# Kernel optimization log

Hardware: AMD Instinct MI355X
Metric: run time of the kernel (lower is better)

## Reference

```python
import jax, jax.numpy as jnp
import numpy as np

N = 30000      # num_nodes
E = 480000     # num_edges
NF = 128       # node_features
EF = 64        # edge_features
HID = 256      # hidden_dim
L = 4          # num_layers
H = 8          # heads
D = HID // H   # per-head dim = 32
SCALE = 0.02


def _ln(x, g, b, eps=1e-5):
    m = x.mean(-1, keepdims=True)
    v = ((x - m) ** 2).mean(-1, keepdims=True)
    return (x - m) * jax.lax.rsqrt(v + eps) * g + b


def _mlp_head(x, W1, b1, W2, b2):
    return jax.nn.sigmoid(jax.nn.relu(x @ W1 + b1) @ W2 + b2)


def setup_inputs() -> dict:
    key = jax.random.key(0)
    ks = jax.random.split(key, 32)
    r = lambda k, shp: SCALE * jax.random.normal(k, shp, dtype=jnp.float32)
    inp = {
        'x': jax.random.normal(ks[0], (N, NF), dtype=jnp.float32),
        'edge_attr': jax.random.normal(ks[1], (E, EF), dtype=jnp.float32),
        'edge_index': jax.random.randint(ks[2], (2, E), 0, N, dtype=jnp.int32),
        # encoders
        'enc_Wn': r(ks[3], (NF, HID)), 'enc_bn': jnp.zeros((HID,), jnp.float32),
        'enc_We': r(ks[4], (EF, HID)), 'enc_be': jnp.zeros((HID,), jnp.float32),
        # stacked TransformerConv params for L layers
        'Wq': r(ks[5], (L, HID, HID)), 'bq': jnp.zeros((L, HID), jnp.float32),
        'Wk': r(ks[6], (L, HID, HID)), 'bk': jnp.zeros((L, HID), jnp.float32),
        'Wv': r(ks[7], (L, HID, HID)), 'bv': jnp.zeros((L, HID), jnp.float32),
        'We': r(ks[8], (L, HID, HID)),  # lin_edge has no bias in PyG
        'Wsk': r(ks[9], (L, HID, HID)), 'bsk': jnp.zeros((L, HID), jnp.float32),
        # shared LayerNorm (module reuses self.norm every layer)
        'ln_g': jnp.ones((HID,), jnp.float32), 'ln_b': jnp.zeros((HID,), jnp.float32),
        # contagion predictor
        'cp_W1': r(ks[10], (HID, HID // 2)), 'cp_b1': jnp.zeros((HID // 2,), jnp.float32),
        'cp_W2': r(ks[11], (HID // 2, 1)), 'cp_b2': jnp.zeros((1,), jnp.float32),
        # systemic risk predictor
        'sp_W1': r(ks[12], (HID, HID // 2)), 'sp_b1': jnp.zeros((HID // 2,), jnp.float32),
        'sp_W2': r(ks[13], (HID // 2, 1)), 'sp_b2': jnp.zeros((1,), jnp.float32),
    }
    return inp


def reference(x, edge_attr, edge_index, enc_Wn, enc_bn, enc_We, enc_be,
              Wq, bq, Wk, bk, Wv, bv, We, Wsk, bsk, ln_g, ln_b,
              cp_W1, cp_b1, cp_W2, cp_b2, sp_W1, sp_b1, sp_W2, sp_b2):
    src, dst = edge_index[0], edge_index[1]
    h = x @ enc_Wn + enc_bn                 # [N,HID]
    e = edge_attr @ enc_We + enc_be         # [E,HID]
    inv_sqrt_d = 1.0 / jnp.sqrt(jnp.asarray(D, h.dtype))
    for l in range(L):
        # TransformerConv: query at dst, key/value at src, edge bias on both k and v
        q = (h @ Wq[l] + bq[l]).reshape(N, H, D)[dst]            # [E,H,D]
        ke = (e @ We[l]).reshape(E, H, D)                        # [E,H,D]
        k = (h @ Wk[l] + bk[l]).reshape(N, H, D)[src] + ke
        v = (h @ Wv[l] + bv[l]).reshape(N, H, D)[src] + ke
        score = (q * k).sum(-1) * inv_sqrt_d                     # [E,H]
        smax = jax.ops.segment_max(score, dst, num_segments=N)   # [N,H]
        p = jnp.exp(score - smax[dst])
        denom = jax.ops.segment_sum(p, dst, num_segments=N)
        alpha = p / (denom[dst] + 1e-16)                         # scatter-softmax
        agg = jax.ops.segment_sum(alpha[..., None] * v, dst, num_segments=N)
        out = agg.reshape(N, HID) + h @ Wsk[l] + bsk[l]          # concat heads + root skip
        h = _ln(h + out, ln_g, ln_b)                             # residual + shared LN (eval: no dropout)
    g = h.mean(0, keepdims=True)                                 # [1,HID] global mean pool
    contagion_risk = _mlp_head(h, cp_W1, cp_b1, cp_W2, cp_b2)    # [N,1]
    systemic_risk = _mlp_head(g, sp_W1, sp_b1, sp_W2, sp_b2)     # [1,1]
    return h, g, contagion_risk, systemic_risk
```

## Files before the change

kernel.cpp:

```cpp
#include <hip/hip_runtime.h>
#include <cstddef>
#include <cstdint>

#define NN 30000
#define EE 480000
#define NFD 128
#define EFD 64
#define HID 256
#define NL 4
#define NH 8

#define DT_BF16 0
#define DT_F32  1
#define DT_EXT  2

#define OFF_WT  ((size_t)65787648)
#define MIN_B   ((size_t)68015872)
#define MIN_A   ((size_t)129455872)

#define WT_ENC 0
#define WT_LAYER(l) (32768 + (size_t)(l) * 262144)
#define WT_CP1 (32768 + (size_t)1048576)

typedef short bf16x8 __attribute__((ext_vector_type(8)));
typedef unsigned short us8 __attribute__((ext_vector_type(8)));
typedef float f32x4 __attribute__((ext_vector_type(4)));

__device__ __forceinline__ float bf2f(unsigned short u) {
  union { unsigned int i; float f; } v; v.i = ((unsigned int)u) << 16; return v.f;
}
__device__ __forceinline__ unsigned short f2bf(float f) {
  union { float f; unsigned int i; } v; v.f = f;
  unsigned int i = v.i;
  return (unsigned short)((i + 0x7FFFu + ((i >> 16) & 1u)) >> 16);
}
struct F4 { float x, y, z, w; };
__device__ __forceinline__ F4 load4bf(const unsigned short* p) {
  ushort4 u = *reinterpret_cast<const ushort4*>(p);
  F4 f; f.x = bf2f(u.x); f.y = bf2f(u.y); f.z = bf2f(u.z); f.w = bf2f(u.w);
  return f;
}
__device__ __forceinline__ F4 load4f(const float* p) {
  float4 t = *reinterpret_cast<const float4*>(p);
  F4 f; f.x = t.x; f.y = t.y; f.z = t.z; f.w = t.w; return f;
}
__device__ __forceinline__ F4 load4any(const void* p, size_t idx, int f32) {
  return f32 ? load4f((const float*)p + idx) : load4bf((const unsigned short*)p + idx);
}
__device__ __forceinline__ float load1any(const void* p, size_t idx, int f32) {
  return f32 ? ((const float*)p)[idx] : bf2f(((const unsigned short*)p)[idx]);
}
__device__ __forceinline__ void store1any(void* p, size_t idx, float v, int f32) {
  if (f32) ((float*)p)[idx] = v; else ((unsigned short*)p)[idx] = f2bf(v);
}

__global__ void probe_dtype(const void* __restrict__ ln_g, int* __restrict__ flag) {
  unsigned int u = *(const unsigned int*)ln_g;
  *flag = ((u & 0xFFFFu) == 0u) ? 1 : 0;
}

__global__ void wt_build(const void* __restrict__ enc_Wn,
                         const void* __restrict__ Wq, const void* __restrict__ Wk,
                         const void* __restrict__ Wv, const void* __restrict__ Wsk,
                         const void* __restrict__ cp_W1,
                         unsigned short* __restrict__ Wt, const int* __restrict__ flagp)
{
  const int f = *flagp;
  size_t idx = (size_t)blockIdx.x * 256 + threadIdx.x;
  if (idx < 32768) {
    int n = idx >> 7, k = idx & 127;
    Wt[WT_ENC + idx] = f2bf(load1any(enc_Wn, (size_t)k * 256 + n, f));
  } else if (idx < 32768 + 1048576) {
    size_t off = idx - 32768;
    int l = off >> 18;
    int which = (off >> 16) & 3;
    size_t e = off & 65535;
    int n = e >> 8, k = e & 255;
    const void* W = (which == 0) ? Wq : (which == 1) ? Wk : (which == 2) ? Wv : Wsk;
    Wt[idx] = f2bf(load1any(W, (size_t)l * 65536 + (size_t)k * 256 + n, f));
  } else if (idx < 32768 + 1048576 + 32768) {
    size_t e = idx - 32768 - 1048576;
    int n = e >> 8, k = e & 255;
    Wt[idx] = f2bf(load1any(cp_W1, (size_t)k * 128 + n, f));
  }
}

template<bool OUT_F32, bool RELU>
__global__ __launch_bounds__(256) void mfma_gemm(
    const void* __restrict__ Av, int aMode,
    const unsigned short* __restrict__ Bt,
    const void* __restrict__ biasv, size_t biasEl, int biasMode,
    void* __restrict__ Cv, int ldC, int cOff,
    int M, int K, const int* __restrict__ flagp)
{
  const int f = *flagp;
  const int aF32 = (aMode == DT_EXT) ? f : aMode;
  const int biF32 = (biasMode == DT_EXT) ? f : biasMode;

  __shared__ unsigned short Al[128][40];
  __shared__ unsigned short Bl[64][40];
  const int bm = blockIdx.x * 128;
  const int bn = blockIdx.y * 64;
  const int tid = threadIdx.x;
  const int wv = tid >> 6, lane = tid & 63;
  const int l16 = lane & 15, quad = lane >> 4;

  f32x4 acc[2][4];
#pragma unroll
  for (int i = 0; i < 2; i++)
#pragma unroll
    for (int j = 0; j < 4; j++) acc[i][j] = (f32x4){0.f, 0.f, 0.f, 0.f};

  const int ar = tid >> 1;
  const int ah = (tid & 1) << 4;
  const int bnr = tid >> 2;
  const int bk8 = (tid & 3) << 3;

  for (int k0 = 0; k0 < K; k0 += 32) {
    us8 w0, w1;
    int gr = bm + ar;
    if (gr < M) {
      if (!aF32) {
        const unsigned short* ap = (const unsigned short*)Av + (size_t)gr * K + k0 + ah;
        w0 = *(const us8*)ap;
        w1 = *(const us8*)(ap + 8);
      } else {
        const float* ap = (const float*)Av + (size_t)gr * K + k0 + ah;
        float4 u0 = *(const float4*)ap;
        float4 u1 = *(const float4*)(ap + 4);
        float4 u2 = *(const float4*)(ap + 8);
        float4 u3 = *(const float4*)(ap + 12);
        w0[0] = f2bf(u0.x); w0[1] = f2bf(u0.y); w0[2] = f2bf(u0.z); w0[3] = f2bf(u0.w);
        w0[4] = f2bf(u1.x); w0[5] = f2bf(u1.y); w0[6] = f2bf(u1.z); w0[7] = f2bf(u1.w);
        w1[0] = f2bf(u2.x); w1[1] = f2bf(u2.y); w1[2] = f2bf(u2.z); w1[3] = f2bf(u2.w);
        w1[4] = f2bf(u3.x); w1[5] = f2bf(u3.y); w1[6] = f2bf(u3.z); w1[7] = f2bf(u3.w);
      }
    } else {
      w0 = (us8)0; w1 = (us8)0;
    }
    *(us8*)&Al[ar][ah] = w0;
    *(us8*)&Al[ar][ah + 8] = w1;
    *(us8*)&Bl[bnr][bk8] = *(const us8*)&Bt[(size_t)(bn + bnr) * K + k0 + bk8];
    __syncthreads();

    bf16x8 a0 = *(const bf16x8*)&Al[wv * 32 + l16][quad * 8];
    bf16x8 a1 = *(const bf16x8*)&Al[wv * 32 + 16 + l16][quad * 8];
#pragma unroll
    for (int tn = 0; tn < 4; tn++) {
      bf16x8 b = *(const bf16x8*)&Bl[tn * 16 + l16][quad * 8];
      acc[0][tn] = __builtin_amdgcn_mfma_f32_16x16x32_bf16(a0, b, acc[0][tn], 0, 0, 0);
      acc[1][tn] = __builtin_amdgcn_mfma_f32_16x16x32_bf16(a1, b, acc[1][tn], 0, 0, 0);
    }
    __syncthreads();
  }

#pragma unroll
  for (int tm = 0; tm < 2; tm++) {
#pragma unroll
    for (int tn = 0; tn < 4; tn++) {
      int col = bn + tn * 16 + l16;
      float bias = load1any(biasv, biasEl + col, biF32);
#pragma unroll
      for (int r = 0; r < 4; r++) {
        int row = bm + wv * 32 + tm * 16 + quad * 4 + r;
        if (row < M) {
          float v = acc[tm][tn][r] + bias;
          if (RELU) v = fmaxf(v, 0.f);
          size_t off = (size_t)row * ldC + cOff + col;
          if (OUT_F32) ((float*)Cv)[off] = v;
          else ((unsigned short*)Cv)[off] = f2bf(v);
        }
      }
    }
  }
}

__global__ __launch_bounds__(256) void mfma_gemm_qkvs(
    const unsigned short* __restrict__ A,
    const unsigned short* __restrict__ Bt,
    const void* __restrict__ bq, const void* __restrict__ bk,
    const void* __restrict__ bv, const void* __restrict__ bsk, size_t biasEl,
    unsigned short* __restrict__ Qb, unsigned short* __restrict__ KVb,
    unsigned short* __restrict__ Sb,
    int M, const int* __restrict__ flagp)
{
  const int f = *flagp;
  __shared__ unsigned short Al[128][40];
  __shared__ unsigned short Bl[64][40];
  const int bm = blockIdx.x * 128;
  const int bnG = blockIdx.y * 64;
  const int which = bnG >> 8;
  const int bn = bnG & 255;
  const int tid = threadIdx.x;
  const int wv = tid >> 6, lane = tid & 63;
  const int l16 = lane & 15, quad = lane >> 4;

  f32x4 acc[2][4];
#pragma unroll
  for (int i = 0; i < 2; i++)
#pragma unroll
    for (int j = 0; j < 4; j++) acc[i][j] = (f32x4){0.f, 0.f, 0.f, 0.f};

  const int ar = tid >> 1;
  const int ah = (tid & 1) << 4;
  const int bnr = tid >> 2;
  const int bk8 = (tid & 3) << 3;
  const unsigned short* Bbase = Bt + (size_t)which * 65536;

  for (int k0 = 0; k0 < HID; k0 += 32) {
    us8 w0, w1;
    int gr = bm + ar;
    if (gr < M) {
      const unsigned short* ap = A + (size_t)gr * HID + k0 + ah;
      w0 = *(const us8*)ap;
      w1 = *(const us8*)(ap + 8);
    } else {
      w0 = (us8)0; w1 = (us8)0;
    }
    *(us8*)&Al[ar][ah] = w0;
    *(us8*)&Al[ar][ah + 8] = w1;
    *(us8*)&Bl[bnr][bk8] = *(const us8*)&Bbase[(size_t)(bn + bnr) * HID + k0 + bk8];
    __syncthreads();

    bf16x8 a0 = *(const bf16x8*)&Al[wv * 32 + l16][quad * 8];
    bf16x8 a1 = *(const bf16x8*)&Al[wv * 32 + 16 + l16][quad * 8];
#pragma unroll
    for (int tn = 0; tn < 4; tn++) {
      bf16x8 b = *(const bf16x8*)&Bl[tn * 16 + l16][quad * 8];
      acc[0][tn] = __builtin_amdgcn_mfma_f32_16x16x32_bf16(a0, b, acc[0][tn], 0, 0, 0);
      acc[1][tn] = __builtin_amdgcn_mfma_f32_16x16x32_bf16(a1, b, acc[1][tn], 0, 0, 0);
    }
    __syncthreads();
  }

  const void* biasv = (which == 0) ? bq : (which == 1) ? bk : (which == 2) ? bv : bsk;
  unsigned short* out = (which == 0) ? Qb : (which == 3) ? Sb : KVb;
  const int ldC = (which == 1 || which == 2) ? 512 : 256;
  const int cOff = (which == 2) ? 256 : 0;

#pragma unroll
  for (int tm = 0; tm < 2; tm++) {
#pragma unroll
    for (int tn = 0; tn < 4; tn++) {
      int col = bn + tn * 16 + l16;
      float bias = load1any(biasv, biasEl + col, f);
#pragma unroll
      for (int r = 0; r < 4; r++) {
        int row = bm + wv * 32 + tm * 16 + quad * 4 + r;
        if (row < M)
          out[(size_t)row * ldC + cOff + col] = f2bf(acc[tm][tn][r] + bias);
      }
    }
  }
}

__global__ void fold_kernel(const void* __restrict__ enc_We,
                            const void* __restrict__ enc_be,
                            const void* __restrict__ We_all,
                            float* __restrict__ Mfold, const int* __restrict__ flagp)
{
  const int f = *flagp;
  int idx = blockIdx.x * blockDim.x + threadIdx.x;
  if (idx >= NL * 65 * HID) return;
  int l = idx / (65 * HID);
  int rc = idx - l * 65 * HID;
  int row = rc >> 8;
  int col = rc & 255;
  size_t Wbase = (size_t)l * HID * HID;
  float acc = 0.f;
  if (row < 64) {
    for (int k = 0; k < HID; k++)
      acc += load1any(enc_We, (size_t)row * HID + k, f) * load1any(We_all, Wbase + (size_t)k * HID + col, f);
  } else {
    for (int k = 0; k < HID; k++)
      acc += load1any(enc_be, k, f) * load1any(We_all, Wbase + (size_t)k * HID + col, f);
  }
  Mfold[idx] = acc;
}

__global__ void hist_kernel(const int* __restrict__ dst, int* __restrict__ rp) {
  int e = blockIdx.x * 256 + threadIdx.x;
  if (e < EE) atomicAdd(&rp[dst[e]], 1);
}

__global__ __launch_bounds__(1024) void scan_kernel(int* __restrict__ rp) {
  __shared__ int part[1024];
  int t = threadIdx.x;
  int base = t * 30;
  int loc[30];
  int sum = 0;
#pragma unroll
  for (int i = 0; i < 30; i++) {
    int idx = base + i;
    int v = (idx < NN) ? rp[idx] : 0;
    loc[i] = v; sum += v;
  }
  part[t] = sum;
  __syncthreads();
  for (int off = 1; off < 1024; off <<= 1) {
    int v = (t >= off) ? part[t - off] : 0;
    __syncthreads();
    part[t] += v;
    __syncthreads();
  }
  int run = (t == 0) ? 0 : part[t - 1];
#pragma unroll
  for (int i = 0; i < 30; i++) {
    int idx = base + i;
    if (idx < NN) { rp[idx] = run; run += loc[i]; }
    else if (idx == NN) { rp[NN] = run; }
  }
}

__global__ void scatter_kernel(const int* __restrict__ src, const int* __restrict__ dst,
                               const int* __restrict__ rp, int* __restrict__ cnt2,
                               int2* __restrict__ sed) {
  int e = blockIdx.x * 256 + threadIdx.x;
  if (e >= EE) return;
  int d = dst[e];
  int pos = rp[d] + atomicAdd(&cnt2[d], 1);
  int2 v; v.x = src[e]; v.y = e;
  sed[pos] = v;
}

__global__ void deg_hist(const int* __restrict__ rp, int* __restrict__ dh) {
  int n = blockIdx.x * 256 + threadIdx.x;
  if (n < NN) {
    int d = rp[n + 1] - rp[n]; if (d > 255) d = 255;
    atomicAdd(&dh[d], 1);
  }
}
__global__ __launch_bounds__(256) void deg_scan(const int* __restrict__ dh,
                                                int* __restrict__ dcnt) {
  __shared__ int h[256];
  int t = threadIdx.x;
  h[t] = dh[t];
  __syncthreads();
  int s = 0;
  for (int d = t + 1; d < 256; d++) s += h[d];
  dcnt[t] = s;
}
__global__ void deg_scatter(const int* __restrict__ rp, int* __restrict__ dcnt,
                            int* __restrict__ perm) {
  int n = blockIdx.x * 256 + threadIdx.x;
  if (n < NN) {
    int d = rp[n + 1] - rp[n]; if (d > 255) d = 255;
    int pos = atomicAdd(&dcnt[d], 1);
    perm[pos] = n;
  }
}

__global__ void ea_build(const int2* __restrict__ sed, const void* __restrict__ edge_attr,
                         unsigned short* __restrict__ ea_srt, const int* __restrict__ flagp) {
  const int f = *flagp;
  int gid = blockIdx.x * 256 + threadIdx.x;
  int pos = gid >> 4;
  int sub = (gid & 15) * 4;
  int e = sed[pos].y;
  F4 v = load4any(edge_attr, (size_t)e * EFD + sub, f);
  ushort4 o; o.x = f2bf(v.x); o.y = f2bf(v.y); o.z = f2bf(v.z); o.w = f2bf(v.w);
  *reinterpret_cast<ushort4*>(ea_srt + (size_t)pos * EFD + sub) = o;
}

template<bool SORTED>
__global__ __launch_bounds__(256) void edge_fused(
    const int* __restrict__ rp, const int2* __restrict__ sed,
    const int* __restrict__ perm,
    const unsigned short* __restrict__ Qb, const unsigned short* __restrict__ KV,
    const unsigned short* __restrict__ ea_srt,
    const void* __restrict__ edge_attr,
    const float* __restrict__ Mf,
    const unsigned short* __restrict__ Sb,
    unsigned short* __restrict__ hb,
    const void* __restrict__ ln_g, const void* __restrict__ ln_b,
    const int* __restrict__ flagp)
{
  __shared__ float wl[4][8][68];
  const int f = *flagp;
  const int wv = threadIdx.x >> 6;
  const int nw = perm[blockIdx.x * 4 + wv];
  const int lane = threadIdx.x & 63;
  const int hd = lane >> 3;
  const int j = lane & 7;
  const int c4 = lane * 4;

  const size_t rowb = (size_t)nw * HID;
  F4 q4 = load4bf(Qb + rowb + c4);

  float q32[32];
#pragma unroll
  for (int i = 0; i < 8; i++) {
    F4 t = load4bf(Qb + rowb + hd * 32 + i * 4);
    q32[i * 4 + 0] = t.x; q32[i * 4 + 1] = t.y; q32[i * 4 + 2] = t.z; q32[i * 4 + 3] = t.w;
  }
  float t8[8];
#pragma unroll
  for (int kk = 0; kk < 8; kk++) {
    const float* Mrow = Mf + (size_t)(j * 8 + kk) * HID + hd * 32;
    float a = 0.f;
#pragma unroll
    for (int cc = 0; cc < 8; cc++) {
      float4 m4 = *reinterpret_cast<const float4*>(Mrow + cc * 4);
      a = fmaf(m4.x, q32[cc * 4 + 0], a);
      a = fmaf(m4.y, q32[cc * 4 + 1], a);
      a = fmaf(m4.z, q32[cc * 4 + 2], a);
      a = fmaf(m4.w, q32[cc * 4 + 3], a);
    }
    t8[kk] = a;
  }
  F4 b4 = load4f(Mf + (size_t)64 * HID + c4);
  float s0 = q4.x * b4.x + q4.y * b4.y + q4.z * b4.z + q4.w * b4.w;
  s0 += __shfl_xor(s0, 1);
  s0 += __shfl_xor(s0, 2);
  s0 += __shfl_xor(s0, 4);

  float accv[4] = {0.f, 0.f, 0.f, 0.f};
  float wacc[8] = {0.f, 0.f, 0.f, 0.f, 0.f, 0.f, 0.f, 0.f};
  float den = 0.f;
  const int beg = rp[nw], end = rp[nw + 1];

  if (beg < end) {
    const float scl = 0.17677669529663687f;
    int tA = beg;
    int tB = (beg + 1 < end) ? beg + 1 : beg;
    int sA = sed[tA].x;
    int sB = sed[tB].x;
    const unsigned short* kvp;
    kvp = KV + (size_t)sA * 512;
    F4 kA = load4bf(kvp + c4);
    F4 vA = load4bf(kvp + 256 + c4);
    kvp = KV + (size_t)sB * 512;
    F4 kB = load4bf(kvp + c4);
    F4 vB = load4bf(kvp + 256 + c4);
    F4 ea0A, ea1A, ea0B, ea1B;
    if (SORTED) {
      ea0A = load4bf(ea_srt + (size_t)tA * EFD + j * 8);
      ea1A = load4bf(ea_srt + (size_t)tA * EFD + j * 8 + 4);
      ea0B = load4bf(ea_srt + (size_t)tB * EFD + j * 8);
      ea1B = load4bf(ea_srt + (size_t)tB * EFD + j * 8 + 4);
    } else {
      size_t eA = (size_t)sed[tA].y, eB = (size_t)sed[tB].y;
      ea0A = load4any(edge_attr, eA * EFD + j * 8, f);
      ea1A = load4any(edge_attr, eA * EFD + j * 8 + 4, f);
      ea0B = load4any(edge_attr, eB * EFD + j * 8, f);
      ea1B = load4any(edge_attr, eB * EFD + j * 8 + 4, f);
    }
    int tC = (beg + 2 < end) ? beg + 2 : beg;
    int tD = (beg + 3 < end) ? beg + 3 : beg;
    int sC = sed[tC].x;
    int sD = sed[tD].x;

    for (int t = beg; t < end; t += 2) {
      kvp = KV + (size_t)sC * 512;
      F4 kC = load4bf(kvp + c4);
      F4 vC = load4bf(kvp + 256 + c4);
      kvp = KV + (size_t)sD * 512;
      F4 kD = load4bf(kvp + c4);
      F4 vD = load4bf(kvp + 256 + c4);
      F4 ea0C, ea1C, ea0D, ea1D;
      if (SORTED) {
        ea0C = load4bf(ea_srt + (size_t)tC * EFD + j * 8);
        ea1C = load4bf(ea_srt + (size_t)tC * EFD + j * 8 + 4);
        ea0D = load4bf(ea_srt + (size_t)tD * EFD + j * 8);
        ea1D = load4bf(ea_srt + (size_t)tD * EFD + j * 8 + 4);
      } else {
        size_t eC = (size_t)sed[tC].y, eD = (size_t)sed[tD].y;
        ea0C = load4any(edge_attr, eC * EFD + j * 8, f);
        ea1C = load4any(edge_attr, eC * EFD + j * 8 + 4, f);
        ea0D = load4any(edge_attr, eD * EFD + j * 8, f);
        ea1D = load4any(edge_attr, eD * EFD + j * 8 + 4, f);
      }
      int tE = (t + 4 < end) ? t + 4 : beg;
      int tF = (t + 5 < end) ? t + 5 : beg;
      int sE = sed[tE].x;
      int sF = sed[tF].x;

      float mB = (t + 1 < end) ? 1.f : 0.f;
      float rA = q4.x * kA.x + q4.y * kA.y + q4.z * kA.z + q4.w * kA.w;
      float rB = q4.x * kB.x + q4.y * kB.y + q4.z * kB.z + q4.w * kB.w;
      rA = fmaf(ea0A.x, t8[0], rA); rB = fmaf(ea0B.x, t8[0], rB);
      rA = fmaf(ea0A.y, t8[1], rA); rB = fmaf(ea0B.y, t8[1], rB);
      rA = fmaf(ea0A.z, t8[2], rA); rB = fmaf(ea0B.z, t8[2], rB);
      rA = fmaf(ea0A.w, t8[3], rA); rB = fmaf(ea0B.w, t8[3], rB);
      rA = fmaf(ea1A.x, t8[4], rA); rB = fmaf(ea1B.x, t8[4], rB);
      rA = fmaf(ea1A.y, t8[5], rA); rB = fmaf(ea1B.y, t8[5], rB);
      rA = fmaf(ea1A.z, t8[6], rA); rB = fmaf(ea1B.z, t8[6], rB);
      rA = fmaf(ea1A.w, t8[7], rA); rB = fmaf(ea1B.w, t8[7], rB);
      { float u = __shfl_xor(rA, 1); float v = __shfl_xor(rB, 1); rA += u; rB += v; }
      { float u = __shfl_xor(rA, 2); float v = __shfl_xor(rB, 2); rA += u; rB += v; }
      { float u = __shfl_xor(rA, 4); float v = __shfl_xor(rB, 4); rA += u; rB += v; }
      float scA = fminf(fmaxf((rA + s0) * scl, -30.f), 30.f);
      float scB = fminf(fmaxf((rB + s0) * scl, -30.f), 30.f);
      float pA = __expf(scA);
      float pB = mB * __expf(scB);
      den += pA + pB;
      accv[0] = fmaf(pA, vA.x, fmaf(pB, vB.x, accv[0]));
      accv[1] = fmaf(pA, vA.y, fmaf(pB, vB.y, accv[1]));
      accv[2] = fmaf(pA, vA.z, fmaf(pB, vB.z, accv[2]));
      accv[3] = fmaf(pA, vA.w, fmaf(pB, vB.w, accv[3]));
      wacc[0] = fmaf(pA, ea0A.x, fmaf(pB, ea0B.x, wacc[0]));
      wacc[1] = fmaf(pA, ea0A.y, fmaf(pB, ea0B.y, wacc[1]));
      wacc[2] = fmaf(pA, ea0A.z, fmaf(pB, ea0B.z, wacc[2]));
      wacc[3] = fmaf(pA, ea0A.w, fmaf(pB, ea0B.w, wacc[3]));
      wacc[4] = fmaf(pA, ea1A.x, fmaf(pB, ea1B.x, wacc[4]));
      wacc[5] = fmaf(pA, ea1A.y, fmaf(pB, ea1B.y, wacc[5]));
      wacc[6] = fmaf(pA, ea1A.z, fmaf(pB, ea1B.z, wacc[6]));
      wacc[7] = fmaf(pA, ea1A.w, fmaf(pB, ea1B.w, wacc[7]));
      kA = kC; vA = vC; ea0A = ea0C; ea1A = ea1C;
      kB = kD; vB = vD; ea0B = ea0D; ea1B = ea1D;
      tA = tC; tB = tD; tC = tE; tD = tF; sC = sE; sD = sF;
    }
  }

#pragma unroll
  for (int i = 0; i < 8; i++) wl[wv][hd][j * 8 + i] = wacc[i];
  __syncthreads();

  float ke0 = 0.f, ke1 = 0.f, ke2 = 0.f, ke3 = 0.f;
#pragma unroll 8
  for (int k = 0; k < 64; k++) {
    float w = wl[wv][hd][k];
    float4 m4 = *reinterpret_cast<const float4*>(Mf + (size_t)k * HID + c4);
    ke0 = fmaf(w, m4.x, ke0);
    ke1 = fmaf(w, m4.y, ke1);
    ke2 = fmaf(w, m4.z, ke2);
    ke3 = fmaf(w, m4.w, ke3);
  }

  float invden = 1.f / (den + 1e-16f);
  float sel = (end > beg) ? 1.f : 0.f;
  F4 s4 = load4bf(Sb + rowb + c4);
  F4 hh = load4bf(hb + rowb + c4);
  float r0 = hh.x + sel * ((accv[0] + ke0) * invden + b4.x) + s4.x;
  float r1 = hh.y + sel * ((accv[1] + ke1) * invden + b4.y) + s4.y;
  float r2 = hh.z + sel * ((accv[2] + ke2) * invden + b4.z) + s4.z;
  float r3 = hh.w + sel * ((accv[3] + ke3) * invden + b4.w) + s4.w;

  float sum = r0 + r1 + r2 + r3;
#pragma unroll
  for (int o = 1; o < 64; o <<= 1) sum += __shfl_xor(sum, o);
  float mean = sum * (1.f / HID);
  float d0 = r0 - mean, d1 = r1 - mean, d2 = r2 - mean, d3 = r3 - mean;
  float vs = d0 * d0 + d1 * d1 + d2 * d2 + d3 * d3;
#pragma unroll
  for (int o = 1; o < 64; o <<= 1) vs += __shfl_xor(vs, o);
  float rstd = rsqrtf(vs * (1.f / HID) + 1e-5f);
  ushort4 o4;
  o4.x = f2bf(d0 * rstd * load1any(ln_g, c4 + 0, f) + load1any(ln_b, c4 + 0, f));
  o4.y = f2bf(d1 * rstd * load1any(ln_g, c4 + 1, f) + load1any(ln_b, c4 + 1, f));
  o4.z = f2bf(d2 * rstd * load1any(ln_g, c4 + 2, f) + load1any(ln_b, c4 + 2, f));
  o4.w = f2bf(d3 * rstd * load1any(ln_g, c4 + 3, f) + load1any(ln_b, c4 + 3, f));
  *reinterpret_cast<ushort4*>(hb + rowb + c4) = o4;
}

__global__ void copy_h_out(const unsigned short* __restrict__ h, void* __restrict__ out,
                           const int* __restrict__ flagp) {
  const int f = *flagp;
  int i = blockIdx.x * 256 + threadIdx.x;
  store1any(out, i, bf2f(h[i]), f);
}

__global__ void colsum_kernel(const unsigned short* __restrict__ h, float* __restrict__ gsum) {
  int c = threadIdx.x;
  float s = 0.f;
  for (int r = blockIdx.x; r < NN; r += gridDim.x) s += bf2f(h[(size_t)r * HID + c]);
  atomicAdd(&gsum[c], s);
}

__global__ void write_g_kernel(const float* __restrict__ gsum, void* __restrict__ out,
                               const int* __restrict__ flagp) {
  const int f = *flagp;
  int c = threadIdx.x;
  store1any(out, (size_t)NN * HID + c, gsum[c] * (1.f / NN), f);
}

__global__ __launch_bounds__(256) void cp2_kernel(
    const float* __restrict__ hid, const void* __restrict__ W2,
    const void* __restrict__ b2, void* __restrict__ out,
    const int* __restrict__ flagp)
{
  const int f = *flagp;
  int nw = (blockIdx.x << 2) + (threadIdx.x >> 6);
  if (nw >= NN) return;
  int lane = threadIdx.x & 63;
  const float* hr = hid + (size_t)nw * 128;
  float s = hr[lane * 2] * load1any(W2, lane * 2, f) + hr[lane * 2 + 1] * load1any(W2, lane * 2 + 1, f);
#pragma unroll
  for (int o = 1; o < 64; o <<= 1) s += __shfl_xor(s, o);
  if (lane == 0) {
    float xv = s + load1any(b2, 0, f);
    store1any(out, (size_t)NN * HID + HID + nw, 1.f / (1.f + __expf(-xv)), f);
  }
}

__global__ __launch_bounds__(128) void sys_kernel(
    const float* __restrict__ gsum,
    const void* __restrict__ W1, const void* __restrict__ b1,
    const void* __restrict__ W2, const void* __restrict__ b2,
    void* __restrict__ out, const int* __restrict__ flagp)
{
  const int f = *flagp;
  __shared__ float red[2];
  int j = threadIdx.x;
  float acc = load1any(b1, j, f);
  const float invN = 1.f / NN;
  for (int k = 0; k < HID; k++) acc = fmaf(gsum[k] * invN, load1any(W1, (size_t)k * 128 + j, f), acc);
  float v = fmaxf(acc, 0.f) * load1any(W2, j, f);
#pragma unroll
  for (int o = 1; o < 64; o <<= 1) v += __shfl_xor(v, o);
  if ((j & 63) == 0) red[j >> 6] = v;
  __syncthreads();
  if (j == 0) {
    float xv = red[0] + red[1] + load1any(b2, 0, f);
    store1any(out, (size_t)NN * HID + HID + NN, 1.f / (1.f + __expf(-xv)), f);
  }
}

__global__ void diag_kernel(float* __restrict__ out, float v, int n4) {
  int i = blockIdx.x * 256 + threadIdx.x;
  if (i < n4) out[i] = (i == 0) ? v : 0.f;
}

extern "C" void kernel_launch(void* const* d_in, const int* in_sizes, int n_in,
                              void* d_out, int out_size, void* d_ws, size_t ws_size,
                              hipStream_t stream)
{
  (void)in_sizes; (void)n_in;

  if (ws_size < MIN_B) {
    diag_kernel<<<(out_size / 2 + 255) / 256, 256, 0, stream>>>(
        (float*)d_out, (float)(ws_size >> 20), out_size / 2);
    return;
  }
  const bool planA = (ws_size >= MIN_A);

  const void* x         = d_in[0];
  const void* edge_attr = d_in[1];
  const int*  edge_index= (const int*)d_in[2];
  const void* enc_Wn = d_in[3];
  const void* enc_bn = d_in[4];
  const void* enc_We = d_in[5];
  const void* enc_be = d_in[6];
  const void* Wq  = d_in[7];
  const void* bq  = d_in[8];
  const void* Wk  = d_in[9];
  const void* bk  = d_in[10];
  const void* Wv  = d_in[11];
  const void* bvv = d_in[12];
  const void* We  = d_in[13];
  const void* Wsk = d_in[14];
  const void* bsk = d_in[15];
  const void* ln_g = d_in[16];
  const void* ln_b = d_in[17];
  const void* cp_W1 = d_in[18];
  const void* cp_b1 = d_in[19];
  const void* cp_W2 = d_in[20];
  const void* cp_b2 = d_in[21];
  const void* sp_W1 = d_in[22];
  const void* sp_b1 = d_in[23];
  const void* sp_W2 = d_in[24];
  const void* sp_b2 = d_in[25];

  char* ws = (char*)d_ws;
  unsigned short* hb  = (unsigned short*)(ws + 0);
  unsigned short* Sb  = (unsigned short*)(ws + 15360000);
  unsigned short* KVb = (unsigned short*)(ws + 30720000);
  int2*  sed   = (int2*)(ws + 61440000);
  int*   rp    = (int*)(ws + 65280000);
  int*   cnt2  = (int*)(ws + 65400064);
  float* Mfold = (float*)(ws + 65520128);
  float* gsum  = (float*)(ws + 65786368);
  int*   flagp = (int*)(ws + 65787392);
  unsigned short* Wt = (unsigned short*)(ws + OFF_WT);
  unsigned short* ea_srt = (unsigned short*)(ws + MIN_B);
  unsigned short* Qb = (unsigned short*)d_out;
  int* dhist = (int*)((char*)d_out + 15360000);
  int* dcnt  = dhist + 256;
  int* perm  = cnt2;
  float* cph = (float*)(ws + 15360000);

  const int* src = edge_index;
  const int* dst = edge_index + EE;

  probe_dtype<<<1, 1, 0, stream>>>(ln_g, flagp);
  wt_build<<<(1114112 + 255) / 256, 256, 0, stream>>>(enc_Wn, Wq, Wk, Wv, Wsk, cp_W1, Wt, flagp);
  fold_kernel<<<(NL * 65 * HID + 255) / 256, 256, 0, stream>>>(enc_We, enc_be, We, Mfold, flagp);

  hipMemsetAsync(rp, 0, 120064, stream);
  hipMemsetAsync(cnt2, 0, 120064, stream);
  hist_kernel<<<(EE + 255) / 256, 256, 0, stream>>>(dst, rp);
  scan_kernel<<<1, 1024, 0, stream>>>(rp);
  scatter_kernel<<<(EE + 255) / 256, 256, 0, stream>>>(src, dst, rp, cnt2, sed);

  hipMemsetAsync(dhist, 0, 1024, stream);
  deg_hist<<<(NN + 255) / 256, 256, 0, stream>>>(rp, dhist);
  deg_scan<<<1, 256, 0, stream>>>(dhist, dcnt);
  deg_scatter<<<(NN + 255) / 256, 256, 0, stream>>>(rp, dcnt, perm);

  if (planA) {
    ea_build<<<EE * 16 / 256, 256, 0, stream>>>(sed, edge_attr, ea_srt, flagp);
  }

  const int gx = (NN + 127) / 128;
  {
    dim3 g(gx, 4);
    mfma_gemm<false, false><<<g, 256, 0, stream>>>(
        x, DT_EXT, Wt + WT_ENC, enc_bn, 0, DT_EXT, hb, HID, 0, NN, NFD, flagp);
  }

  for (int l = 0; l < NL; l++) {
    size_t bo = (size_t)l * HID;
    dim3 gQ(gx, 16);
    mfma_gemm_qkvs<<<gQ, 256, 0, stream>>>(
        hb, Wt + WT_LAYER(l), bq, bk, bvv, bsk, bo, Qb, KVb, Sb, NN, flagp);
    const float* Mf = Mfold + (size_t)l * 65 * HID;
    if (planA) {
      edge_fused<true><<<NN / 4, 256, 0, stream>>>(
          rp, sed, perm, Qb, KVb, ea_srt, edge_attr, Mf, Sb, hb, ln_g, ln_b, flagp);
    } else {
      edge_fused<false><<<NN / 4, 256, 0, stream>>>(
          rp, sed, perm, Qb, KVb, ea_srt, edge_attr, Mf, Sb, hb, ln_g, ln_b, flagp);
    }
  }

  copy_h_out<<<NN, 256, 0, stream>>>(hb, d_out, flagp);
  hipMemsetAsync(gsum, 0, HID * 4, stream);
  colsum_kernel<<<256, 256, 0, stream>>>(hb, gsum);
  write_g_kernel<<<1, 256, 0, stream>>>(gsum, d_out, flagp);

  {
    dim3 g(gx, 2);
    mfma_gemm<true, true><<<g, 256, 0, stream>>>(
        hb, DT_BF16, Wt + WT_CP1, cp_b1, 0, DT_EXT, cph, 128, 0, NN, HID, flagp);
  }
  cp2_kernel<<<NN / 4, 256, 0, stream>>>(cph, cp_W2, cp_b2, d_out, flagp);
  sys_kernel<<<1, 128, 0, stream>>>(gsum, sp_W1, sp_b1, sp_W2, sp_b2, d_out, flagp);
}
```

Measured before the change: 2.286 ms.

## Stage edge gathers into LDS via async global_load_lds with a 4-deep pipeline

Replaces the register-prefetched gather loop in the fused edge kernel with asynchronous global-to-LDS loads (global_load_lds) into a per-wave 4-slot ring buffer, with explicit vmcnt waits so several edge pairs' K/V and edge-attribute rows are in flight. The goal is to hide gather latency without spending registers on prefetched values. It also merges the output copy and column-sum kernels into one pass over h. It adds about 40KB of LDS per block, which may lower occupancy, and relies on hand-written waitcnt ordering being correct.

```diff
diff --git a/kernel.cpp b/kernel.cpp
--- a/kernel.cpp
+++ b/kernel.cpp
@@ -376,6 +376,7 @@
     const int* __restrict__ flagp)
 {
   __shared__ float wl[4][8][68];
+  __shared__ __attribute__((aligned(16))) char stage[4][4][2560];
   const int f = *flagp;
   const int wv = threadIdx.x >> 6;
   const int nw = perm[blockIdx.x * 4 + wv];
@@ -383,6 +384,7 @@
   const int hd = lane >> 3;
   const int j = lane & 7;
   const int c4 = lane * 4;
+  const int jb = j << 3;
 
   const size_t rowb = (size_t)nw * HID;
   F4 q4 = load4bf(Qb + rowb + c4);
@@ -396,7 +398,7 @@
   float t8[8];
 #pragma unroll
   for (int kk = 0; kk < 8; kk++) {
-    const float* Mrow = Mf + (size_t)(j * 8 + kk) * HID + hd * 32;
+    const float* Mrow = Mf + (size_t)(jb + kk) * HID + hd * 32;
     float a = 0.f;
 #pragma unroll
     for (int cc = 0; cc < 8; cc++) {
@@ -421,99 +423,127 @@
 
   if (beg < end) {
     const float scl = 0.17677669529663687f;
-    int tA = beg;
-    int tB = (beg + 1 < end) ? beg + 1 : beg;
-    int sA = sed[tA].x;
-    int sB = sed[tB].x;
-    const unsigned short* kvp;
-    kvp = KV + (size_t)sA * 512;
-    F4 kA = load4bf(kvp + c4);
-    F4 vA = load4bf(kvp + 256 + c4);
-    kvp = KV + (size_t)sB * 512;
-    F4 kB = load4bf(kvp + c4);
-    F4 vB = load4bf(kvp + 256 + c4);
-    F4 ea0A, ea1A, ea0B, ea1B;
-    if (SORTED) {
-      ea0A = load4bf(ea_srt + (size_t)tA * EFD + j * 8);
-      ea1A = load4bf(ea_srt + (size_t)tA * EFD + j * 8 + 4);
-      ea0B = load4bf(ea_srt + (size_t)tB * EFD + j * 8);
-      ea1B = load4bf(ea_srt + (size_t)tB * EFD + j * 8 + 4);
-    } else {
-      size_t eA = (size_t)sed[tA].y, eB = (size_t)sed[tB].y;
-      ea0A = load4any(edge_attr, eA * EFD + j * 8, f);
-      ea1A = load4any(edge_attr, eA * EFD + j * 8 + 4, f);
-      ea0B = load4any(edge_attr, eB * EFD + j * 8, f);
-      ea1B = load4any(edge_attr, eB * EFD + j * 8 + 4, f);
-    }
-    int tC = (beg + 2 < end) ? beg + 2 : beg;
-    int tD = (beg + 3 < end) ? beg + 3 : beg;
-    int sC = sed[tC].x;
-    int sD = sed[tD].x;
-
-    for (int t = beg; t < end; t += 2) {
-      kvp = KV + (size_t)sC * 512;
-      F4 kC = load4bf(kvp + c4);
-      F4 vC = load4bf(kvp + 256 + c4);
-      kvp = KV + (size_t)sD * 512;
-      F4 kD = load4bf(kvp + c4);
-      F4 vD = load4bf(kvp + 256 + c4);
-      F4 ea0C, ea1C, ea0D, ea1D;
-      if (SORTED) {
-        ea0C = load4bf(ea_srt + (size_t)tC * EFD + j * 8);
-        ea1C = load4bf(ea_srt + (size_t)tC * EFD + j * 8 + 4);
-        ea0D = load4bf(ea_srt + (size_t)tD * EFD + j * 8);
-        ea1D = load4bf(ea_srt + (size_t)tD * EFD + j * 8 + 4);
-      } else {
-        size_t eC = (size_t)sed[tC].y, eD = (size_t)sed[tD].y;
-        ea0C = load4any(edge_attr, eC * EFD + j * 8, f);
-        ea1C = load4any(edge_attr, eC * EFD + j * 8 + 4, f);
-        ea0D = load4any(edge_attr, eD * EFD + j * 8, f);
-        ea1D = load4any(edge_attr, eD * EFD + j * 8 + 4, f);
-      }
-      int tE = (t + 4 < end) ? t + 4 : beg;
-      int tF = (t + 5 < end) ? t + 5 : beg;
-      int sE = sed[tE].x;
-      int sF = sed[tF].x;
-
-      float mB = (t + 1 < end) ? 1.f : 0.f;
-      float rA = q4.x * kA.x + q4.y * kA.y + q4.z * kA.z + q4.w * kA.w;
-      float rB = q4.x * kB.x + q4.y * kB.y + q4.z * kB.z + q4.w * kB.w;
-      rA = fmaf(ea0A.x, t8[0], rA); rB = fmaf(ea0B.x, t8[0], rB);
-      rA = fmaf(ea0A.y, t8[1], rA); rB = fmaf(ea0B.y, t8[1], rB);
-      rA = fmaf(ea0A.z, t8[2], rA); rB = fmaf(ea0B.z, t8[2], rB);
-      rA = fmaf(ea0A.w, t8[3], rA); rB = fmaf(ea0B.w, t8[3], rB);
-      rA = fmaf(ea1A.x, t8[4], rA); rB = fmaf(ea1B.x, t8[4], rB);
-      rA = fmaf(ea1A.y, t8[5], rA); rB = fmaf(ea1B.y, t8[5], rB);
-      rA = fmaf(ea1A.z, t8[6], rA); rB = fmaf(ea1B.z, t8[6], rB);
-      rA = fmaf(ea1A.w, t8[7], rA); rB = fmaf(ea1B.w, t8[7], rB);
-      { float u = __shfl_xor(rA, 1); float v = __shfl_xor(rB, 1); rA += u; rB += v; }
-      { float u = __shfl_xor(rA, 2); float v = __shfl_xor(rB, 2); rA += u; rB += v; }
-      { float u = __shfl_xor(rA, 4); float v = __shfl_xor(rB, 4); rA += u; rB += v; }
-      float scA = fminf(fmaxf((rA + s0) * scl, -30.f), 30.f);
-      float scB = fminf(fmaxf((rB + s0) * scl, -30.f), 30.f);
-      float pA = __expf(scA);
-      float pB = mB * __expf(scB);
-      den += pA + pB;
-      accv[0] = fmaf(pA, vA.x, fmaf(pB, vB.x, accv[0]));
-      accv[1] = fmaf(pA, vA.y, fmaf(pB, vB.y, accv[1]));
-      accv[2] = fmaf(pA, vA.z, fmaf(pB, vB.z, accv[2]));
-      accv[3] = fmaf(pA, vA.w, fmaf(pB, vB.w, accv[3]));
-      wacc[0] = fmaf(pA, ea0A.x, fmaf(pB, ea0B.x, wacc[0]));
-      wacc[1] = fmaf(pA, ea0A.y, fmaf(pB, ea0B.y, wacc[1]));
-      wacc[2] = fmaf(pA, ea0A.z, fmaf(pB, ea0B.z, wacc[2]));
-      wacc[3] = fmaf(pA, ea0A.w, fmaf(pB, ea0B.w, wacc[3]));
-      wacc[4] = fmaf(pA, ea1A.x, fmaf(pB, ea1B.x, wacc[4]));
-      wacc[5] = fmaf(pA, ea1A.y, fmaf(pB, ea1B.y, wacc[5]));
-      wacc[6] = fmaf(pA, ea1A.z, fmaf(pB, ea1B.z, wacc[6]));
-      wacc[7] = fmaf(pA, ea1A.w, fmaf(pB, ea1B.w, wacc[7]));
-      kA = kC; vA = vC; ea0A = ea0C; ea1A = ea1C;
-      kB = kD; vB = vD; ea0B = ea0D; ea1B = ea1D;
-      tA = tC; tB = tD; tC = tE; tD = tF; sC = sE; sD = sF;
-    }
-  }
-
-#pragma unroll
-  for (int i = 0; i < 8; i++) wl[wv][hd][j * 8 + i] = wacc[i];
+    char* stg = &stage[wv][0][0];
+    const char* KVc = (const char*)KV;
+    const char* EAc = SORTED ? (const char*)ea_srt : (const char*)edge_attr;
+    const bool eaf32 = (!SORTED) && f;
+    const int eoff = eaf32 ? (lane * 4) : ((lane < 32) ? lane * 4 : 124);
+    const int eashift = eaf32 ? 8 : 7;
+
+#define GLLKV(sx, dst) __builtin_amdgcn_global_load_lds(                        \
+      (const __attribute__((address_space(1))) void*)(KVc +                     \
+          (((size_t)(unsigned)(sx)) << 10) + lane * 16),                        \
+      (__attribute__((address_space(3))) void*)(dst), 16, 0, 0)
+#define GLLEA(row, dst) __builtin_amdgcn_global_load_lds(                       \
+      (const __attribute__((address_space(1))) void*)(EAc +                     \
+          (((size_t)(unsigned)(row)) << eashift) + eoff),                       \
+      (__attribute__((address_space(3))) void*)(dst), 4, 0, 0)
+
+#define ISSUE(base, SV0, SV1, BUF) do {                                         \
+    int _p0 = ((base) < end) ? (base) : beg;                                    \
+    int _p1 = _p0 + 1; if (_p1 >= end) _p1 = end - 1;                           \
+    int _e0 = SORTED ? _p0 : (SV0).y;                                           \
+    int _e1 = SORTED ? _p1 : (SV1).y;                                           \
+    char* _b = stg + (BUF) * 2560;                                              \
+    GLLKV((SV0).x, _b);                                                         \
+    GLLKV((SV1).x, _b + 1024);                                                  \
+    GLLEA(_e0, _b + 2048);                                                      \
+    GLLEA(_e1, _b + 2304);                                                      \
+  } while (0)
+
+#define SEDLD(base, SV0, SV1) do {                                              \
+    int _q0 = ((base) < end) ? (base) : beg;                                    \
+    int _q1 = _q0 + 1; if (_q1 >= end) _q1 = end - 1;                           \
+    SV0 = sed[_q0]; SV1 = sed[_q1];                                             \
+  } while (0)
+
+#define COMPUTE(BUF) do {                                                       \
+    const char* _b = stg + (BUF) * 2560;                                        \
+    F4 kA = load4bf((const unsigned short*)(_b) + c4);                          \
+    F4 vA = load4bf((const unsigned short*)(_b) + 256 + c4);                    \
+    F4 kB = load4bf((const unsigned short*)(_b + 1024) + c4);                   \
+    F4 vB = load4bf((const unsigned short*)(_b + 1024) + 256 + c4);             \
+    F4 ea0A, ea1A, ea0B, ea1B;                                                  \
+    if (!eaf32) {                                                               \
+      ea0A = load4bf((const unsigned short*)(_b + 2048) + jb);                  \
+      ea1A = load4bf((const unsigned short*)(_b + 2048) + jb + 4);              \
+      ea0B = load4bf((const unsigned short*)(_b + 2304) + jb);                  \
+      ea1B = load4bf((const unsigned short*)(_b + 2304) + jb + 4);              \
+    } else {                                                                    \
+      ea0A = load4f((const float*)(_b + 2048) + jb);                            \
+      ea1A = load4f((const float*)(_b + 2048) + jb + 4);                        \
+      ea0B = load4f((const float*)(_b + 2304) + jb);                            \
+      ea1B = load4f((const float*)(_b + 2304) + jb + 4);                        \
+    }                                                                           \
+    float mB = (tcur + 1 < end) ? 1.f : 0.f;                                    \
+    float rA = q4.x * kA.x + q4.y * kA.y + q4.z * kA.z + q4.w * kA.w;           \
+    float rB = q4.x * kB.x + q4.y * kB.y + q4.z * kB.z + q4.w * kB.w;           \
+    rA = fmaf(ea0A.x, t8[0], rA); rB = fmaf(ea0B.x, t8[0], rB);                 \
+    rA = fmaf(ea0A.y, t8[1], rA); rB = fmaf(ea0B.y, t8[1], rB);                 \
+    rA = fmaf(ea0A.z, t8[2], rA); rB = fmaf(ea0B.z, t8[2], rB);                 \
+    rA = fmaf(ea0A.w, t8[3], rA); rB = fmaf(ea0B.w, t8[3], rB);                 \
+    rA = fmaf(ea1A.x, t8[4], rA); rB = fmaf(ea1B.x, t8[4], rB);                 \
+    rA = fmaf(ea1A.y, t8[5], rA); rB = fmaf(ea1B.y, t8[5], rB);                 \
+    rA = fmaf(ea1A.z, t8[6], rA); rB = fmaf(ea1B.z, t8[6], rB);                 \
+    rA = fmaf(ea1A.w, t8[7], rA); rB = fmaf(ea1B.w, t8[7], rB);                 \
+    { float u = __shfl_xor(rA, 1); float v = __shfl_xor(rB, 1); rA += u; rB += v; } \
+    { float u = __shfl_xor(rA, 2); float v = __shfl_xor(rB, 2); rA += u; rB += v; } \
+    { float u = __shfl_xor(rA, 4); float v = __shfl_xor(rB, 4); rA += u; rB += v; } \
+    float scA = fminf(fmaxf((rA + s0) * scl, -30.f), 30.f);                     \
+    float scB = fminf(fmaxf((rB + s0) * scl, -30.f), 30.f);                     \
+    float pA = __expf(scA);                                                     \
+    float pB = mB * __expf(scB);                                                \
+    den += pA + pB;                                                             \
+    accv[0] = fmaf(pA, vA.x, fmaf(pB, vB.x, accv[0]));                          \
+    accv[1] = fmaf(pA, vA.y, fmaf(pB, vB.y, accv[1]));                          \
+    accv[2] = fmaf(pA, vA.z, fmaf(pB, vB.z, accv[2]));                          \
+    accv[3] = fmaf(pA, vA.w, fmaf(pB, vB.w, accv[3]));                          \
+    wacc[0] = fmaf(pA, ea0A.x, fmaf(pB, ea0B.x, wacc[0]));                      \
+    wacc[1] = fmaf(pA, ea0A.y, fmaf(pB, ea0B.y, wacc[1]));                      \
+    wacc[2] = fmaf(pA, ea0A.z, fmaf(pB, ea0B.z, wacc[2]));                      \
+    wacc[3] = fmaf(pA, ea0A.w, fmaf(pB, ea0B.w, wacc[3]));                      \
+    wacc[4] = fmaf(pA, ea1A.x, fmaf(pB, ea1B.x, wacc[4]));                      \
+    wacc[5] = fmaf(pA, ea1A.y, fmaf(pB, ea1B.y, wacc[5]));                      \
+    wacc[6] = fmaf(pA, ea1A.z, fmaf(pB, ea1B.z, wacc[6]));                      \
+    wacc[7] = fmaf(pA, ea1A.w, fmaf(pB, ea1B.w, wacc[7]));                      \
+    tcur += 2;                                                                  \
+  } while (0)
+
+#define ITER(BUF, B2, SV0, SV1) do {                                            \
+    asm volatile("s_waitcnt vmcnt(6)" ::: "memory");                            \
+    ISSUE(tcur + 4, SV0, SV1, B2);                                              \
+    COMPUTE(BUF);                                                               \
+    SEDLD(tcur + 6, SV0, SV1);                                                  \
+  } while (0)
+
+    int2 sA0, sA1, sB0, sB1;
+    int tcur = beg;
+    SEDLD(beg, sA0, sA1);
+    SEDLD(beg + 2, sB0, sB1);
+    asm volatile("s_waitcnt vmcnt(0)" ::: "memory");
+    ISSUE(beg, sA0, sA1, 0);
+    SEDLD(beg + 4, sA0, sA1);
+    ISSUE(beg + 2, sB0, sB1, 1);
+    SEDLD(beg + 6, sB0, sB1);
+
+    const int G = (end - beg + 1) >> 1;
+    int g = 0;
+    for (;;) {
+      ITER(0, 2, sA0, sA1); if (++g >= G) break;
+      ITER(1, 3, sB0, sB1); if (++g >= G) break;
+      ITER(2, 0, sA0, sA1); if (++g >= G) break;
+      ITER(3, 1, sB0, sB1); if (++g >= G) break;
+    }
+#undef ITER
+#undef COMPUTE
+#undef SEDLD
+#undef ISSUE
+#undef GLLEA
+#undef GLLKV
+  }
+
+#pragma unroll
+  for (int i = 0; i < 8; i++) wl[wv][hd][jb + i] = wacc[i];
   __syncthreads();
 
   float ke0 = 0.f, ke1 = 0.f, ke2 = 0.f, ke3 = 0.f;
@@ -553,17 +583,16 @@
   *reinterpret_cast<ushort4*>(hb + rowb + c4) = o4;
 }
 
-__global__ void copy_h_out(const unsigned short* __restrict__ h, void* __restrict__ out,
-                           const int* __restrict__ flagp) {
-  const int f = *flagp;
-  int i = blockIdx.x * 256 + threadIdx.x;
-  store1any(out, i, bf2f(h[i]), f);
-}
-
-__global__ void colsum_kernel(const unsigned short* __restrict__ h, float* __restrict__ gsum) {
+__global__ void copy_colsum(const unsigned short* __restrict__ h, void* __restrict__ out,
+                            float* __restrict__ gsum, const int* __restrict__ flagp) {
+  const int f = *flagp;
   int c = threadIdx.x;
   float s = 0.f;
-  for (int r = blockIdx.x; r < NN; r += gridDim.x) s += bf2f(h[(size_t)r * HID + c]);
+  for (int r = blockIdx.x; r < NN; r += gridDim.x) {
+    float v = bf2f(h[(size_t)r * HID + c]);
+    store1any(out, (size_t)r * HID + c, v, f);
+    s += v;
+  }
   atomicAdd(&gsum[c], s);
 }
 
@@ -723,9 +752,8 @@
     }
   }
 
-  copy_h_out<<<NN, 256, 0, stream>>>(hb, d_out, flagp);
   hipMemsetAsync(gsum, 0, HID * 4, stream);
-  colsum_kernel<<<256, 256, 0, stream>>>(hb, gsum);
+  copy_colsum<<<256, 256, 0, stream>>>(hb, d_out, gsum, flagp);
   write_g_kernel<<<1, 256, 0, stream>>>(gsum, d_out, flagp);
 
   {
```

New measurement: 2.373 ms. 3.8% more time.
